# Kernel optimization log

Hardware: AMD Instinct MI355X
Metric: run time of the kernel (lower is better)

The kernel has to match this reference:

```python
import jax, jax.numpy as jnp
import numpy as np

B, C, T = 256, 1, 16384   # batch, input_channels, seq_len
H = C                      # hidden_size == input_channels in this module
OUT = 1                    # output_channels


def setup_inputs() -> dict:
    key = jax.random.key(0)
    ks = jax.random.split(key, 11)
    # PyTorch GRU/Linear init: uniform(-1/sqrt(H), 1/sqrt(H)); H=1 -> (-1, 1)
    u = lambda k, shape, s=1.0: jax.random.uniform(k, shape, jnp.float32, -s, s)
    s_lin = 1.0 / np.sqrt(2 * H).astype(np.float32)
    return {
        "x": jax.random.normal(ks[0], (B, C, T), jnp.float32),
        # layer 0: input size C, per direction [3H, C] / [3H, H] / [3H]
        "w_ih0": u(ks[1], (2, 3 * H, C)),
        "w_hh0": u(ks[2], (2, 3 * H, H)),
        "b_ih0": u(ks[3], (2, 3 * H)),
        "b_hh0": u(ks[4], (2, 3 * H)),
        # layers 1-2: input size 2H (bidirectional concat)
        "w_ih12": u(ks[5], (2, 2, 3 * H, 2 * H)),
        "w_hh12": u(ks[6], (2, 2, 3 * H, H)),
        "b_ih12": u(ks[7], (2, 2, 3 * H)),
        "b_hh12": u(ks[8], (2, 2, 3 * H)),
        # output projection Linear(2H -> OUT)
        "w_out": u(ks[9], (OUT, 2 * H), s_lin),
        "b_out": u(ks[10], (OUT,), s_lin),
    }


def _gru_dir(xs, w_ih, w_hh, b_ih, b_hh, reverse):
    """One GRU direction. xs: [T, B, in] -> ys: [T, B, H] (time-aligned)."""
    h0 = jnp.zeros((xs.shape[1], w_hh.shape[1]), xs.dtype)

    def step(h, x_t):
        gi = x_t @ w_ih.T + b_ih          # [B, 3H]
        gh = h @ w_hh.T + b_hh            # [B, 3H]
        ir, iz, inn = jnp.split(gi, 3, axis=-1)
        hr, hz, hn = jnp.split(gh, 3, axis=-1)
        r = jax.nn.sigmoid(ir + hr)
        z = jax.nn.sigmoid(iz + hz)
        n = jnp.tanh(inn + r * hn)
        h_new = (1.0 - z) * n + z * h
        return h_new, h_new

    _, ys = jax.lax.scan(step, h0, xs, reverse=reverse)
    return ys


def _bidir(xs, w_ih_f, w_hh_f, b_ih_f, b_hh_f, w_ih_b, w_hh_b, b_ih_b, b_hh_b):
    fwd = _gru_dir(xs, w_ih_f, w_hh_f, b_ih_f, b_hh_f, reverse=False)
    bwd = _gru_dir(xs, w_ih_b, w_hh_b, b_ih_b, b_hh_b, reverse=True)
    return jnp.concatenate([fwd, bwd], axis=-1)  # [T, B, 2H]


def reference(x, w_ih0, w_hh0, b_ih0, b_hh0, w_ih12, w_hh12, b_ih12, b_hh12, w_out, b_out):
    xs = jnp.transpose(x, (2, 0, 1))  # [B, C, T] -> [T, B, C]
    xs = _bidir(xs, w_ih0[0], w_hh0[0], b_ih0[0], b_hh0[0],
                w_ih0[1], w_hh0[1], b_ih0[1], b_hh0[1])
    for l in range(2):  # GRU layers 1 and 2 (structurally distinct weights)
        xs = _bidir(xs, w_ih12[l, 0], w_hh12[l, 0], b_ih12[l, 0], b_hh12[l, 0],
                    w_ih12[l, 1], w_hh12[l, 1], b_ih12[l, 1], b_hh12[l, 1])
    y = xs @ w_out.T + b_out          # [T, B, OUT]
    return jnp.transpose(y, (1, 2, 0))  # [B, OUT, T]
```

## Files before the change

kernel.cpp:

```cpp
#include <hip/hip_runtime.h>
#include <hip/hip_fp16.h>

#define T_LEN 16384
#define B_SZ  256
#define S_CH  256
#define CL    (T_LEN / S_CH)
#define HALO  32
#define SC    16

__device__ __forceinline__ float ex2(float x)  { return __builtin_amdgcn_exp2f(x); }
__device__ __forceinline__ float rcpf(float x) { return __builtin_amdgcn_rcpf(x); }

__device__ __forceinline__ float ld_cvt(const float* p)  { return *p; }
__device__ __forceinline__ float ld_cvt(const __half* p) { return __half2float(*p); }
__device__ __forceinline__ void  st_cvt(float* p, float v)  { *p = v; }
__device__ __forceinline__ void  st_cvt(__half* p, float v) { *p = __float2half_rn(v); }

__device__ __forceinline__ float gru_step(float h, float preR, float preZ, float preN,
                                          float UR, float UZ, float UN2, float DN2)
{
    float er  = ex2(fmaf(h, UR, preR));
    float ez  = ex2(fmaf(h, UZ, preZ));
    float r   = rcpf(1.0f + er);
    float z   = rcpf(1.0f + ez);
    float hn2 = fmaf(h, UN2, DN2);
    float en  = ex2(fmaf(r, hn2, preN));
    float n   = fmaf(-2.0f, rcpf(1.0f + en), 1.0f);
    float omz = 1.0f - z;
    float zh  = z * h;
    return fmaf(n, omz, zh);
}

template<bool REV>
__device__ void scan0(const float* __restrict__ x,
                      const float* __restrict__ wih, const float* __restrict__ whh,
                      const float* __restrict__ bih, const float* __restrict__ bhh,
                      __half* __restrict__ out, int b, int s)
{
    const int d = REV ? 1 : 0;
    const float L2E = 1.4426950408889634f;
    const float WR  = -L2E * wih[d*3+0];
    const float WZ  = -L2E * wih[d*3+1];
    const float WN  =  2.0f*L2E * wih[d*3+2];
    const float UR  = -L2E * whh[d*3+0];
    const float UZ  = -L2E * whh[d*3+1];
    const float UN2 =  2.0f*L2E * whh[d*3+2];
    const float CR  = -L2E * (bih[d*3+0] + bhh[d*3+0]);
    const float CZ  = -L2E * (bih[d*3+1] + bhh[d*3+1]);
    const float CN  =  2.0f*L2E * bih[d*3+2];
    const float DN2 =  2.0f*L2E * bhh[d*3+2];

    const int warm   = min(HALO, REV ? (T_LEN - (s + 1) * CL) : (s * CL));
    const int nsteps = warm + CL;
    const int t0     = REV ? ((s + 1) * CL - 1 + warm) : (s * CL - warm);

    const float* row = x + (size_t)b * T_LEN;
    __half* po = out + (REV ? B_SZ : 0) + b;

    float xA[SC], xB[SC];
    float h = 0.0f;

    auto LD = [&](float* F, int base) {
        const float4* p = (const float4*)(row + (REV ? (t0 - base - 15) : (t0 + base)));
        float4 v0 = p[0], v1 = p[1], v2 = p[2], v3 = p[3];
        float lin[16] = { v0.x,v0.y,v0.z,v0.w, v1.x,v1.y,v1.z,v1.w,
                          v2.x,v2.y,v2.z,v2.w, v3.x,v3.y,v3.z,v3.w };
        #pragma unroll
        for (int k = 0; k < 16; ++k) F[k] = REV ? lin[15 - k] : lin[k];
        __builtin_amdgcn_sched_barrier(0);
    };

    auto CS = [&](float* F, int base) {
        float ov[SC];
        #pragma unroll
        for (int k = 0; k < SC; ++k) {
            float xv = F[k];
            h = gru_step(h, fmaf(xv, WR, CR), fmaf(xv, WZ, CZ), fmaf(xv, WN, CN),
                         UR, UZ, UN2, DN2);
            ov[k] = h;
        }
        if (base >= warm) {
            #pragma unroll
            for (int k = 0; k < SC; ++k) {
                int t = REV ? (t0 - (base + k)) : (t0 + (base + k));
                st_cvt(po + t * (2 * B_SZ), ov[k]);
            }
        }
    };

    LD(xA, 0);
    const int nsup = nsteps / SC;
    for (int i = 0; i < nsup; i += 2) {
        LD(xB, min((i + 1) * SC, nsteps - SC));
        CS(xA, i * SC);
        LD(xA, min((i + 2) * SC, nsteps - SC));
        CS(xB, (i + 1) * SC);
    }
}

template<bool REV, typename TIN, typename TOUT>
__device__ void scan12(const TIN* __restrict__ in,
                       const float* __restrict__ wih, const float* __restrict__ whh,
                       const float* __restrict__ bih, const float* __restrict__ bhh,
                       TOUT* __restrict__ out, int b, int s)
{
    const int d = REV ? 1 : 0;
    const float L2E = 1.4426950408889634f;
    const float WR0 = -L2E * wih[(d*3+0)*2+0], WR1 = -L2E * wih[(d*3+0)*2+1];
    const float WZ0 = -L2E * wih[(d*3+1)*2+0], WZ1 = -L2E * wih[(d*3+1)*2+1];
    const float WN0 =  2.0f*L2E * wih[(d*3+2)*2+0], WN1 = 2.0f*L2E * wih[(d*3+2)*2+1];
    const float UR  = -L2E * whh[d*3+0];
    const float UZ  = -L2E * whh[d*3+1];
    const float UN2 =  2.0f*L2E * whh[d*3+2];
    const float CR  = -L2E * (bih[d*3+0] + bhh[d*3+0]);
    const float CZ  = -L2E * (bih[d*3+1] + bhh[d*3+1]);
    const float CN  =  2.0f*L2E * bih[d*3+2];
    const float DN2 =  2.0f*L2E * bhh[d*3+2];

    const int warm   = min(HALO, REV ? (T_LEN - (s + 1) * CL) : (s * CL));
    const int nsteps = warm + CL;
    const int t0     = REV ? ((s + 1) * CL - 1 + warm) : (s * CL - warm);

    const TIN* pf = in + b;
    const TIN* pg = in + B_SZ + b;
    TOUT* po = out + (REV ? B_SZ : 0) + b;

    float fA[SC], gA[SC], fB[SC], gB[SC];
    float h = 0.0f;

#define LD12(F, G, base_) { int base = (base_); \
    _Pragma("unroll") for (int k = 0; k < SC; ++k) { \
      int t = REV ? (t0 - (base + k)) : (t0 + (base + k)); \
      F[k] = ld_cvt(pf + t * (2 * B_SZ)); G[k] = ld_cvt(pg + t * (2 * B_SZ)); } \
    __builtin_amdgcn_sched_barrier(0); }

#define CS12(F, G, base_) { int base = (base_); float ov[SC]; \
    _Pragma("unroll") for (int k = 0; k < SC; ++k) { \
      float a = F[k], c = G[k]; \
      float pr = fmaf(a, WR0, fmaf(c, WR1, CR)); \
      float pz = fmaf(a, WZ0, fmaf(c, WZ1, CZ)); \
      float pn = fmaf(a, WN0, fmaf(c, WN1, CN)); \
      h = gru_step(h, pr, pz, pn, UR, UZ, UN2, DN2); ov[k] = h; } \
    if (base >= warm) { \
      _Pragma("unroll") for (int k = 0; k < SC; ++k) { \
        int t = REV ? (t0 - (base + k)) : (t0 + (base + k)); \
        st_cvt(po + t * (2 * B_SZ), ov[k]); } } }

    LD12(fA, gA, 0);
    const int nsup = nsteps / SC;
    for (int i = 0; i < nsup; i += 2) {
        LD12(fB, gB, min((i + 1) * SC, nsteps - SC));
        CS12(fA, gA, i * SC);
        LD12(fA, gA, min((i + 2) * SC, nsteps - SC));
        CS12(fB, gB, (i + 1) * SC);
    }
#undef LD12
#undef CS12
}

__device__ __forceinline__ void decode_blk(int blk, int tid, int& b, int& s, int& dir)
{
    int xcd = blk & 7;
    int j   = blk >> 3;
    int sl  = j & 31;
    int bg  = (j >> 5) & 3;
    dir     = j >> 7;
    s       = xcd * 32 + sl;
    b       = bg * 64 + tid;
}

__global__ void __launch_bounds__(64) k_scan0g(const float* __restrict__ x,
                                               const float* __restrict__ wih,
                                               const float* __restrict__ whh,
                                               const float* __restrict__ bih,
                                               const float* __restrict__ bhh,
                                               __half* __restrict__ out)
{
    int b, s, dir;
    decode_blk(blockIdx.x, threadIdx.x, b, s, dir);
    if (dir == 0) scan0<false>(x, wih, whh, bih, bhh, out, b, s);
    else          scan0<true >(x, wih, whh, bih, bhh, out, b, s);
}

__global__ void __launch_bounds__(64) k_scan1g(const __half* __restrict__ in,
                                               const float* __restrict__ wih,
                                               const float* __restrict__ whh,
                                               const float* __restrict__ bih,
                                               const float* __restrict__ bhh,
                                               __half* __restrict__ out)
{
    int b, s, dir;
    decode_blk(blockIdx.x, threadIdx.x, b, s, dir);
    if (dir == 0) scan12<false>(in, wih, whh, bih, bhh, out, b, s);
    else          scan12<true >(in, wih, whh, bih, bhh, out, b, s);
}

__global__ void __launch_bounds__(64) k_scan2g(const __half* __restrict__ in,
                                               const float* __restrict__ wih,
                                               const float* __restrict__ whh,
                                               const float* __restrict__ bih,
                                               const float* __restrict__ bhh,
                                               float* __restrict__ out)
{
    int b, s, dir;
    decode_blk(blockIdx.x, threadIdx.x, b, s, dir);
    if (dir == 0) scan12<false>(in, wih, whh, bih, bhh, out, b, s);
    else          scan12<true >(in, wih, whh, bih, bhh, out, b, s);
}

__global__ void __launch_bounds__(256) k_proj(const float* __restrict__ h2,
                                              const float* __restrict__ wo,
                                              const float* __restrict__ bo,
                                              float* __restrict__ y)
{
    __shared__ float tile[64][65];
    const int b0 = (blockIdx.x & 3) * 64;
    const int t0 = (blockIdx.x >> 2) * 64;
    const float wf = wo[0], wb = wo[1], bias = bo[0];
    const int bl = threadIdx.x & 63;
    const int tg = threadIdx.x >> 6;
    #pragma unroll
    for (int i = 0; i < 16; ++i) {
        int tl = tg * 16 + i;
        int t  = t0 + tl;
        float f = h2[(size_t)t * (2 * B_SZ) + b0 + bl];
        float g = h2[(size_t)t * (2 * B_SZ) + B_SZ + b0 + bl];
        tile[bl][tl] = fmaf(wf, f, fmaf(wb, g, bias));
    }
    __syncthreads();
    const int c4 = threadIdx.x & 15;
    const int r  = threadIdx.x >> 4;
    #pragma unroll
    for (int i = 0; i < 4; ++i) {
        int brow = r + 16 * i;
        float4 v = make_float4(tile[brow][c4*4+0], tile[brow][c4*4+1],
                               tile[brow][c4*4+2], tile[brow][c4*4+3]);
        ((float4*)y)[(size_t)(b0 + brow) * (T_LEN / 4) + t0 / 4 + c4] = v;
    }
}

extern "C" void kernel_launch(void* const* d_in, const int* in_sizes, int n_in,
                              void* d_out, int out_size, void* d_ws, size_t ws_size,
                              hipStream_t stream)
{
    (void)in_sizes; (void)n_in; (void)out_size; (void)ws_size;
    const float* x      = (const float*)d_in[0];
    const float* w_ih0  = (const float*)d_in[1];
    const float* w_hh0  = (const float*)d_in[2];
    const float* b_ih0  = (const float*)d_in[3];
    const float* b_hh0  = (const float*)d_in[4];
    const float* w_ih12 = (const float*)d_in[5];
    const float* w_hh12 = (const float*)d_in[6];
    const float* b_ih12 = (const float*)d_in[7];
    const float* b_hh12 = (const float*)d_in[8];
    const float* w_out  = (const float*)d_in[9];
    const float* b_out  = (const float*)d_in[10];
    float* y = (float*)d_out;

    char* ws = (char*)d_ws;
    const size_t NN = (size_t)2 * B_SZ * T_LEN;
    __half* l0out = (__half*)ws;
    __half* l1out = (__half*)(ws + NN * 2);
    float*  l2out = (float*)(ws + NN * 4);

    const int nblk = 8 * S_CH;
    k_scan0g<<<nblk, 64, 0, stream>>>(x,     w_ih0,       w_hh0,      b_ih0,      b_hh0,      l0out);
    k_scan1g<<<nblk, 64, 0, stream>>>(l0out, w_ih12 + 0,  w_hh12 + 0, b_ih12 + 0, b_hh12 + 0, l1out);
    k_scan2g<<<nblk, 64, 0, stream>>>(l1out, w_ih12 + 12, w_hh12 + 6, b_ih12 + 6, b_hh12 + 6, l2out);
    k_proj  <<<1024, 256, 0, stream>>>(l2out, w_out, b_out, y);
}
```

Measured before the change: 135.4 us.

## Fuse GRU layers 1, 2 and output projection into one LDS-staged kernel

```diff
diff --git a/kernel.cpp b/kernel.cpp
--- a/kernel.cpp
+++ b/kernel.cpp
@@ -98,66 +98,6 @@
     }
 }
 
-template<bool REV, typename TIN, typename TOUT>
-__device__ void scan12(const TIN* __restrict__ in,
-                       const float* __restrict__ wih, const float* __restrict__ whh,
-                       const float* __restrict__ bih, const float* __restrict__ bhh,
-                       TOUT* __restrict__ out, int b, int s)
-{
-    const int d = REV ? 1 : 0;
-    const float L2E = 1.4426950408889634f;
-    const float WR0 = -L2E * wih[(d*3+0)*2+0], WR1 = -L2E * wih[(d*3+0)*2+1];
-    const float WZ0 = -L2E * wih[(d*3+1)*2+0], WZ1 = -L2E * wih[(d*3+1)*2+1];
-    const float WN0 =  2.0f*L2E * wih[(d*3+2)*2+0], WN1 = 2.0f*L2E * wih[(d*3+2)*2+1];
-    const float UR  = -L2E * whh[d*3+0];
-    const float UZ  = -L2E * whh[d*3+1];
-    const float UN2 =  2.0f*L2E * whh[d*3+2];
-    const float CR  = -L2E * (bih[d*3+0] + bhh[d*3+0]);
-    const float CZ  = -L2E * (bih[d*3+1] + bhh[d*3+1]);
-    const float CN  =  2.0f*L2E * bih[d*3+2];
-    const float DN2 =  2.0f*L2E * bhh[d*3+2];
-
-    const int warm   = min(HALO, REV ? (T_LEN - (s + 1) * CL) : (s * CL));
-    const int nsteps = warm + CL;
-    const int t0     = REV ? ((s + 1) * CL - 1 + warm) : (s * CL - warm);
-
-    const TIN* pf = in + b;
-    const TIN* pg = in + B_SZ + b;
-    TOUT* po = out + (REV ? B_SZ : 0) + b;
-
-    float fA[SC], gA[SC], fB[SC], gB[SC];
-    float h = 0.0f;
-
-#define LD12(F, G, base_) { int base = (base_); \
-    _Pragma("unroll") for (int k = 0; k < SC; ++k) { \
-      int t = REV ? (t0 - (base + k)) : (t0 + (base + k)); \
-      F[k] = ld_cvt(pf + t * (2 * B_SZ)); G[k] = ld_cvt(pg + t * (2 * B_SZ)); } \
-    __builtin_amdgcn_sched_barrier(0); }
-
-#define CS12(F, G, base_) { int base = (base_); float ov[SC]; \
-    _Pragma("unroll") for (int k = 0; k < SC; ++k) { \
-      float a = F[k], c = G[k]; \
-      float pr = fmaf(a, WR0, fmaf(c, WR1, CR)); \
-      float pz = fmaf(a, WZ0, fmaf(c, WZ1, CZ)); \
-      float pn = fmaf(a, WN0, fmaf(c, WN1, CN)); \
-      h = gru_step(h, pr, pz, pn, UR, UZ, UN2, DN2); ov[k] = h; } \
-    if (base >= warm) { \
-      _Pragma("unroll") for (int k = 0; k < SC; ++k) { \
-        int t = REV ? (t0 - (base + k)) : (t0 + (base + k)); \
-        st_cvt(po + t * (2 * B_SZ), ov[k]); } } }
-
-    LD12(fA, gA, 0);
-    const int nsup = nsteps / SC;
-    for (int i = 0; i < nsup; i += 2) {
-        LD12(fB, gB, min((i + 1) * SC, nsteps - SC));
-        CS12(fA, gA, i * SC);
-        LD12(fA, gA, min((i + 2) * SC, nsteps - SC));
-        CS12(fB, gB, (i + 1) * SC);
-    }
-#undef LD12
-#undef CS12
-}
-
 __device__ __forceinline__ void decode_blk(int blk, int tid, int& b, int& s, int& dir)
 {
     int xcd = blk & 7;
@@ -182,60 +122,173 @@
     else          scan0<true >(x, wih, whh, bih, bhh, out, b, s);
 }
 
-__global__ void __launch_bounds__(64) k_scan1g(const __half* __restrict__ in,
-                                               const float* __restrict__ wih,
-                                               const float* __restrict__ whh,
-                                               const float* __restrict__ bih,
-                                               const float* __restrict__ bhh,
-                                               __half* __restrict__ out)
-{
-    int b, s, dir;
-    decode_blk(blockIdx.x, threadIdx.x, b, s, dir);
-    if (dir == 0) scan12<false>(in, wih, whh, bih, bhh, out, b, s);
-    else          scan12<true >(in, wih, whh, bih, bhh, out, b, s);
-}
-
-__global__ void __launch_bounds__(64) k_scan2g(const __half* __restrict__ in,
-                                               const float* __restrict__ wih,
-                                               const float* __restrict__ whh,
-                                               const float* __restrict__ bih,
-                                               const float* __restrict__ bhh,
-                                               float* __restrict__ out)
-{
-    int b, s, dir;
-    decode_blk(blockIdx.x, threadIdx.x, b, s, dir);
-    if (dir == 0) scan12<false>(in, wih, whh, bih, bhh, out, b, s);
-    else          scan12<true >(in, wih, whh, bih, bhh, out, b, s);
-}
-
-__global__ void __launch_bounds__(256) k_proj(const float* __restrict__ h2,
-                                              const float* __restrict__ wo,
-                                              const float* __restrict__ bo,
-                                              float* __restrict__ y)
-{
-    __shared__ float tile[64][65];
-    const int b0 = (blockIdx.x & 3) * 64;
-    const int t0 = (blockIdx.x >> 2) * 64;
-    const float wf = wo[0], wb = wo[1], bias = bo[0];
-    const int bl = threadIdx.x & 63;
-    const int tg = threadIdx.x >> 6;
-    #pragma unroll
-    for (int i = 0; i < 16; ++i) {
-        int tl = tg * 16 + i;
-        int t  = t0 + tl;
-        float f = h2[(size_t)t * (2 * B_SZ) + b0 + bl];
-        float g = h2[(size_t)t * (2 * B_SZ) + B_SZ + b0 + bl];
-        tile[bl][tl] = fmaf(wf, f, fmaf(wb, g, bias));
+__global__ void __launch_bounds__(128) k12p(const __half* __restrict__ in,
+        const float* __restrict__ w_ih12, const float* __restrict__ w_hh12,
+        const float* __restrict__ b_ih12, const float* __restrict__ b_hh12,
+        const float* __restrict__ wo, const float* __restrict__ bo,
+        float* __restrict__ y)
+{
+    __shared__ __align__(16) char smem[33024];
+    __half (*lds1)[2][64] = reinterpret_cast<__half(*)[2][64]>(smem);
+    float  (*tG)[64]      = reinterpret_cast<float(*)[64]>(smem);
+    float  (*tY)[65]      = reinterpret_cast<float(*)[65]>(smem + 16384);
+
+    const int blk  = blockIdx.x;
+    const int xcd  = blk & 7;
+    const int jj_  = blk >> 3;
+    const int sl   = jj_ & 31;
+    const int bg   = jj_ >> 5;
+    const int s    = xcd * 32 + sl;
+    const int lane = threadIdx.x & 63;
+    const int w    = threadIdx.x >> 6;
+    const int b    = bg * 64 + lane;
+    const int sg   = w ? -1 : 1;
+
+    const int t0     = s * CL;
+    const int warmF2 = min(HALO, t0);
+    const int warmB2 = min(HALO, T_LEN - (t0 + CL));
+    const int a1     = t0 - warmF2;
+    const int e1     = t0 + CL + warmB2;
+    const int L      = e1 - a1;
+
+    const float L2E = 1.4426950408889634f;
+
+    {
+        const int d = w;
+        const float WR0 = -L2E * w_ih12[(d*3+0)*2+0], WR1 = -L2E * w_ih12[(d*3+0)*2+1];
+        const float WZ0 = -L2E * w_ih12[(d*3+1)*2+0], WZ1 = -L2E * w_ih12[(d*3+1)*2+1];
+        const float WN0 =  2.0f*L2E * w_ih12[(d*3+2)*2+0], WN1 = 2.0f*L2E * w_ih12[(d*3+2)*2+1];
+        const float UR  = -L2E * w_hh12[d*3+0];
+        const float UZ  = -L2E * w_hh12[d*3+1];
+        const float UN2 =  2.0f*L2E * w_hh12[d*3+2];
+        const float CR  = -L2E * (b_ih12[d*3+0] + b_hh12[d*3+0]);
+        const float CZ  = -L2E * (b_ih12[d*3+1] + b_hh12[d*3+1]);
+        const float CN  =  2.0f*L2E * b_ih12[d*3+2];
+        const float DN2 =  2.0f*L2E * b_hh12[d*3+2];
+
+        const int warm1   = w ? min(HALO, T_LEN - e1) : min(HALO, a1);
+        const int nsteps1 = warm1 + L;
+        const int tstart1 = w ? (e1 - 1 + warm1) : (a1 - warm1);
+
+        const __half* pf = in + b;
+        const __half* pg = in + B_SZ + b;
+
+        float fA[SC], gA[SC], fB[SC], gB[SC];
+        float h = 0.0f;
+
+#define LD1(F, G, base_) { int base = (base_); \
+    _Pragma("unroll") for (int k = 0; k < SC; ++k) { \
+      int t = tstart1 + sg * (base + k); \
+      F[k] = ld_cvt(pf + t * (2 * B_SZ)); G[k] = ld_cvt(pg + t * (2 * B_SZ)); } \
+    __builtin_amdgcn_sched_barrier(0); }
+
+#define CS1(F, G, base_) { int base = (base_); float ov[SC]; \
+    _Pragma("unroll") for (int k = 0; k < SC; ++k) { \
+      float a = F[k], c = G[k]; \
+      float pr = fmaf(a, WR0, fmaf(c, WR1, CR)); \
+      float pz = fmaf(a, WZ0, fmaf(c, WZ1, CZ)); \
+      float pn = fmaf(a, WN0, fmaf(c, WN1, CN)); \
+      h = gru_step(h, pr, pz, pn, UR, UZ, UN2, DN2); ov[k] = h; } \
+    if (base >= warm1) { \
+      _Pragma("unroll") for (int k = 0; k < SC; ++k) { \
+        int t = tstart1 + sg * (base + k); \
+        lds1[t - a1][d][lane] = __float2half_rn(ov[k]); } } }
+
+        LD1(fA, gA, 0);
+        const int nsup = nsteps1 / SC;
+        for (int i = 0; i < nsup; i += 2) {
+            LD1(fB, gB, min((i + 1) * SC, nsteps1 - SC));
+            CS1(fA, gA, i * SC);
+            LD1(fA, gA, min((i + 2) * SC, nsteps1 - SC));
+            CS1(fB, gB, (i + 1) * SC);
+        }
+#undef LD1
+#undef CS1
     }
     __syncthreads();
-    const int c4 = threadIdx.x & 15;
-    const int r  = threadIdx.x >> 4;
-    #pragma unroll
-    for (int i = 0; i < 4; ++i) {
-        int brow = r + 16 * i;
-        float4 v = make_float4(tile[brow][c4*4+0], tile[brow][c4*4+1],
-                               tile[brow][c4*4+2], tile[brow][c4*4+3]);
-        ((float4*)y)[(size_t)(b0 + brow) * (T_LEN / 4) + t0 / 4 + c4] = v;
+
+    float f[CL];
+    {
+        const int d = w;
+        const float* wih2 = w_ih12 + 12;
+        const float* whh2 = w_hh12 + 6;
+        const float* bih2 = b_ih12 + 6;
+        const float* bhh2 = b_hh12 + 6;
+        const float WR0 = -L2E * wih2[(d*3+0)*2+0], WR1 = -L2E * wih2[(d*3+0)*2+1];
+        const float WZ0 = -L2E * wih2[(d*3+1)*2+0], WZ1 = -L2E * wih2[(d*3+1)*2+1];
+        const float WN0 =  2.0f*L2E * wih2[(d*3+2)*2+0], WN1 = 2.0f*L2E * wih2[(d*3+2)*2+1];
+        const float UR  = -L2E * whh2[d*3+0];
+        const float UZ  = -L2E * whh2[d*3+1];
+        const float UN2 =  2.0f*L2E * whh2[d*3+2];
+        const float CR  = -L2E * (bih2[d*3+0] + bhh2[d*3+0]);
+        const float CZ  = -L2E * (bih2[d*3+1] + bhh2[d*3+1]);
+        const float CN  =  2.0f*L2E * bih2[d*3+2];
+        const float DN2 =  2.0f*L2E * bhh2[d*3+2];
+
+        const int warm2 = w ? warmB2 : warmF2;
+        const int idx0  = w ? (L - 1) : 0;
+        float h = 0.0f;
+
+        for (int jj = 0; jj < warm2; jj += SC) {
+            float av[SC], cv[SC];
+            #pragma unroll
+            for (int k = 0; k < SC; ++k) {
+                int idx = idx0 + sg * (jj + k);
+                av[k] = __half2float(lds1[idx][0][lane]);
+                cv[k] = __half2float(lds1[idx][1][lane]);
+            }
+            #pragma unroll
+            for (int k = 0; k < SC; ++k) {
+                float pr = fmaf(av[k], WR0, fmaf(cv[k], WR1, CR));
+                float pz = fmaf(av[k], WZ0, fmaf(cv[k], WZ1, CZ));
+                float pn = fmaf(av[k], WN0, fmaf(cv[k], WN1, CN));
+                h = gru_step(h, pr, pz, pn, UR, UZ, UN2, DN2);
+            }
+        }
+        #pragma unroll
+        for (int q = 0; q < CL / SC; ++q) {
+            float av[SC], cv[SC];
+            #pragma unroll
+            for (int k = 0; k < SC; ++k) {
+                int idx = idx0 + sg * (warm2 + q * SC + k);
+                av[k] = __half2float(lds1[idx][0][lane]);
+                cv[k] = __half2float(lds1[idx][1][lane]);
+            }
+            #pragma unroll
+            for (int k = 0; k < SC; ++k) {
+                float pr = fmaf(av[k], WR0, fmaf(cv[k], WR1, CR));
+                float pz = fmaf(av[k], WZ0, fmaf(cv[k], WZ1, CZ));
+                float pn = fmaf(av[k], WN0, fmaf(cv[k], WN1, CN));
+                h = gru_step(h, pr, pz, pn, UR, UZ, UN2, DN2);
+                f[q * SC + k] = h;
+            }
+        }
+    }
+    __syncthreads();
+
+    if (w == 1) {
+        #pragma unroll
+        for (int m = 0; m < CL; ++m) tG[CL - 1 - m][lane] = f[m];
+    }
+    __syncthreads();
+    if (w == 0) {
+        const float wf = wo[0], wb = wo[1], bias = bo[0];
+        #pragma unroll
+        for (int m = 0; m < CL; ++m)
+            tY[lane][m] = fmaf(wf, f[m], fmaf(wb, tG[m][lane], bias));
+    }
+    __syncthreads();
+    {
+        const int b0 = bg * 64;
+        const int c4 = threadIdx.x & 15;
+        const int r  = (threadIdx.x >> 4) & 7;
+        #pragma unroll
+        for (int i = 0; i < 8; ++i) {
+            int brow = r + 8 * i;
+            float4 v = make_float4(tY[brow][c4*4+0], tY[brow][c4*4+1],
+                                   tY[brow][c4*4+2], tY[brow][c4*4+3]);
+            ((float4*)y)[(size_t)(b0 + brow) * (T_LEN / 4) + (t0 >> 2) + c4] = v;
+        }
     }
 }
 
@@ -257,15 +310,9 @@
     const float* b_out  = (const float*)d_in[10];
     float* y = (float*)d_out;
 
-    char* ws = (char*)d_ws;
-    const size_t NN = (size_t)2 * B_SZ * T_LEN;
-    __half* l0out = (__half*)ws;
-    __half* l1out = (__half*)(ws + NN * 2);
-    float*  l2out = (float*)(ws + NN * 4);
-
-    const int nblk = 8 * S_CH;
-    k_scan0g<<<nblk, 64, 0, stream>>>(x,     w_ih0,       w_hh0,      b_ih0,      b_hh0,      l0out);
-    k_scan1g<<<nblk, 64, 0, stream>>>(l0out, w_ih12 + 0,  w_hh12 + 0, b_ih12 + 0, b_hh12 + 0, l1out);
-    k_scan2g<<<nblk, 64, 0, stream>>>(l1out, w_ih12 + 12, w_hh12 + 6, b_ih12 + 6, b_hh12 + 6, l2out);
-    k_proj  <<<1024, 256, 0, stream>>>(l2out, w_out, b_out, y);
-}
+    __half* l0out = (__half*)d_ws;
+
+    k_scan0g<<<8 * S_CH, 64, 0, stream>>>(x, w_ih0, w_hh0, b_ih0, b_hh0, l0out);
+    k12p   <<<4 * S_CH, 128, 0, stream>>>(l0out, w_ih12, w_hh12, b_ih12, b_hh12,
+                                          w_out, b_out, y);
+}
```

After: 142.1 us. +4.9%, slower.

## Fuse final GRU layer scan with output projection in one kernel

Applied to the files above, without the earlier changes.

```diff
diff --git a/kernel.cpp b/kernel.cpp
--- a/kernel.cpp
+++ b/kernel.cpp
@@ -195,47 +195,108 @@
     else          scan12<true >(in, wih, whh, bih, bhh, out, b, s);
 }
 
-__global__ void __launch_bounds__(64) k_scan2g(const __half* __restrict__ in,
-                                               const float* __restrict__ wih,
-                                               const float* __restrict__ whh,
-                                               const float* __restrict__ bih,
-                                               const float* __restrict__ bhh,
-                                               float* __restrict__ out)
-{
-    int b, s, dir;
-    decode_blk(blockIdx.x, threadIdx.x, b, s, dir);
-    if (dir == 0) scan12<false>(in, wih, whh, bih, bhh, out, b, s);
-    else          scan12<true >(in, wih, whh, bih, bhh, out, b, s);
-}
-
-__global__ void __launch_bounds__(256) k_proj(const float* __restrict__ h2,
-                                              const float* __restrict__ wo,
-                                              const float* __restrict__ bo,
-                                              float* __restrict__ y)
-{
-    __shared__ float tile[64][65];
-    const int b0 = (blockIdx.x & 3) * 64;
-    const int t0 = (blockIdx.x >> 2) * 64;
+__global__ void __launch_bounds__(128) k2p(const __half* __restrict__ in,
+        const float* __restrict__ wih, const float* __restrict__ whh,
+        const float* __restrict__ bih, const float* __restrict__ bhh,
+        const float* __restrict__ wo, const float* __restrict__ bo,
+        float* __restrict__ y)
+{
+    __shared__ float tY[64][65];
+
+    const int blk  = blockIdx.x;
+    const int xcd  = blk & 7;
+    const int jj   = blk >> 3;
+    const int sl   = jj & 31;
+    const int bg   = jj >> 5;
+    const int s    = xcd * 32 + sl;
+    const int lane = threadIdx.x & 63;
+    const int w    = threadIdx.x >> 6;
+    const int b    = bg * 64 + lane;
+    const int sg   = w ? -1 : 1;
+    const int t0   = s * CL;
+
+    const int d = w;
+    const float L2E = 1.4426950408889634f;
+    const float WR0 = -L2E * wih[(d*3+0)*2+0], WR1 = -L2E * wih[(d*3+0)*2+1];
+    const float WZ0 = -L2E * wih[(d*3+1)*2+0], WZ1 = -L2E * wih[(d*3+1)*2+1];
+    const float WN0 =  2.0f*L2E * wih[(d*3+2)*2+0], WN1 = 2.0f*L2E * wih[(d*3+2)*2+1];
+    const float UR  = -L2E * whh[d*3+0];
+    const float UZ  = -L2E * whh[d*3+1];
+    const float UN2 =  2.0f*L2E * whh[d*3+2];
+    const float CR  = -L2E * (bih[d*3+0] + bhh[d*3+0]);
+    const float CZ  = -L2E * (bih[d*3+1] + bhh[d*3+1]);
+    const float CN  =  2.0f*L2E * bih[d*3+2];
+    const float DN2 =  2.0f*L2E * bhh[d*3+2];
+
+    const int warm   = w ? min(HALO, T_LEN - (t0 + CL)) : min(HALO, t0);
+    const int tstart = w ? (t0 + CL - 1 + warm) : (t0 - warm);
+
+    const __half* pf = in + b;
+    const __half* pg = in + B_SZ + b;
+
+    float fA[SC], gA[SC], fB[SC], gB[SC];
+    float f[CL];
+    float h = 0.0f;
+
+#define LD2(F, G, base_) { int base = (base_); \
+    _Pragma("unroll") for (int k = 0; k < SC; ++k) { \
+      int t = tstart + sg * (base + k); \
+      F[k] = __half2float(pf[t * (2 * B_SZ)]); \
+      G[k] = __half2float(pg[t * (2 * B_SZ)]); } \
+    __builtin_amdgcn_sched_barrier(0); }
+
+#define CSB(F, G) { \
+    _Pragma("unroll") for (int k = 0; k < SC; ++k) { \
+      float a = F[k], c = G[k]; \
+      float pr = fmaf(a, WR0, fmaf(c, WR1, CR)); \
+      float pz = fmaf(a, WZ0, fmaf(c, WZ1, CZ)); \
+      float pn = fmaf(a, WN0, fmaf(c, WN1, CN)); \
+      h = gru_step(h, pr, pz, pn, UR, UZ, UN2, DN2); } }
+
+#define CSS(F, G, Q) { \
+    _Pragma("unroll") for (int k = 0; k < SC; ++k) { \
+      float a = F[k], c = G[k]; \
+      float pr = fmaf(a, WR0, fmaf(c, WR1, CR)); \
+      float pz = fmaf(a, WZ0, fmaf(c, WZ1, CZ)); \
+      float pn = fmaf(a, WN0, fmaf(c, WN1, CN)); \
+      h = gru_step(h, pr, pz, pn, UR, UZ, UN2, DN2); \
+      f[(Q) * SC + k] = h; } }
+
+    LD2(fA, gA, 0);
+    if (warm) {
+        LD2(fB, gB, SC);      CSB(fA, gA);
+        LD2(fA, gA, 2 * SC);  CSB(fB, gB);
+    }
+    LD2(fB, gB, warm + SC);      CSS(fA, gA, 0);
+    LD2(fA, gA, warm + 2 * SC);  CSS(fB, gB, 1);
+    LD2(fB, gB, warm + 3 * SC);  CSS(fA, gA, 2);
+                                 CSS(fB, gB, 3);
+#undef LD2
+#undef CSB
+#undef CSS
+
     const float wf = wo[0], wb = wo[1], bias = bo[0];
-    const int bl = threadIdx.x & 63;
-    const int tg = threadIdx.x >> 6;
-    #pragma unroll
-    for (int i = 0; i < 16; ++i) {
-        int tl = tg * 16 + i;
-        int t  = t0 + tl;
-        float f = h2[(size_t)t * (2 * B_SZ) + b0 + bl];
-        float g = h2[(size_t)t * (2 * B_SZ) + B_SZ + b0 + bl];
-        tile[bl][tl] = fmaf(wf, f, fmaf(wb, g, bias));
+    if (w == 0) {
+        #pragma unroll
+        for (int m = 0; m < CL; ++m) tY[lane][m] = fmaf(wf, f[m], bias);
     }
     __syncthreads();
-    const int c4 = threadIdx.x & 15;
-    const int r  = threadIdx.x >> 4;
-    #pragma unroll
-    for (int i = 0; i < 4; ++i) {
-        int brow = r + 16 * i;
-        float4 v = make_float4(tile[brow][c4*4+0], tile[brow][c4*4+1],
-                               tile[brow][c4*4+2], tile[brow][c4*4+3]);
-        ((float4*)y)[(size_t)(b0 + brow) * (T_LEN / 4) + t0 / 4 + c4] = v;
+    if (w == 1) {
+        #pragma unroll
+        for (int m = 0; m < CL; ++m) tY[lane][CL - 1 - m] += wb * f[m];
+    }
+    __syncthreads();
+    {
+        const int b0 = bg * 64;
+        const int c4 = threadIdx.x & 15;
+        const int r  = (threadIdx.x >> 4) & 7;
+        #pragma unroll
+        for (int i = 0; i < 8; ++i) {
+            int brow = r + 8 * i;
+            float4 v = make_float4(tY[brow][c4*4+0], tY[brow][c4*4+1],
+                                   tY[brow][c4*4+2], tY[brow][c4*4+3]);
+            ((float4*)y)[(size_t)(b0 + brow) * (T_LEN / 4) + (t0 >> 2) + c4] = v;
+        }
     }
 }
 
@@ -261,11 +322,10 @@
     const size_t NN = (size_t)2 * B_SZ * T_LEN;
     __half* l0out = (__half*)ws;
     __half* l1out = (__half*)(ws + NN * 2);
-    float*  l2out = (float*)(ws + NN * 4);
 
     const int nblk = 8 * S_CH;
     k_scan0g<<<nblk, 64, 0, stream>>>(x,     w_ih0,       w_hh0,      b_ih0,      b_hh0,      l0out);
     k_scan1g<<<nblk, 64, 0, stream>>>(l0out, w_ih12 + 0,  w_hh12 + 0, b_ih12 + 0, b_hh12 + 0, l1out);
-    k_scan2g<<<nblk, 64, 0, stream>>>(l1out, w_ih12 + 12, w_hh12 + 6, b_ih12 + 6, b_hh12 + 6, l2out);
-    k_proj  <<<1024, 256, 0, stream>>>(l2out, w_out, b_out, y);
-}
+    k2p    <<<4 * S_CH, 128, 0, stream>>>(l1out, w_ih12 + 12, w_hh12 + 6, b_ih12 + 6, b_hh12 + 6,
+                                          w_out, b_out, y);
+}
```

After: 143.1 us. 5.6% more time.
